# Kernel tuning notes

Hardware: AMD Instinct MI355X
Metric: run time of the kernel (lower is better)

## Reference

```python
import jax, jax.numpy as jnp
import numpy as np

B, S, H = 2, 2048, 768
NH, DH = 12, 64  # num_heads, dim_head; inner_dim = NH*DH = H
SCALE = DH ** -0.5


def setup_inputs() -> dict:
    key = jax.random.key(0)
    k1, k2, k3 = jax.random.split(key, 3)
    x = jax.random.normal(k1, (B, S, H), dtype=jnp.float32)
    w_qkv = jax.random.normal(k2, (3 * NH * DH, H), dtype=jnp.float32) * (H ** -0.5)
    w_out = jax.random.normal(k3, (H, NH * DH), dtype=jnp.float32) * ((NH * DH) ** -0.5)
    b_out = jnp.zeros((H,), dtype=jnp.float32)
    return {"x": x, "w_qkv": w_qkv, "w_out": w_out, "b_out": b_out}


def reference(x, w_qkv, w_out, b_out):
    b, s, _ = x.shape
    # qkv linear: [b, s, 3*inner]
    qkv = jnp.einsum('bsh,oh->bso', x, w_qkv)
    # 'b s (qkv l d) -> qkv b l s d'  (l = heads)
    qkv = qkv.reshape(b, s, 3, NH, DH).transpose(2, 0, 3, 1, 4)
    q, k, v = qkv[0], qkv[1], qkv[2]  # each [b, nh, s, dh]
    att = jax.nn.softmax(jnp.einsum('bhxd,bhyd->bhxy', q, k) * SCALE, axis=-1)
    out = jnp.einsum('bhxy,bhyd->bhxd', att, v)  # [b, nh, s, dh]
    out = out.transpose(0, 2, 1, 3).reshape(b, s, NH * DH)  # 'b h l d -> b l (h d)'
    return jnp.einsum('bsi,oi->bso', out, w_out) + b_out
```

## Files before the change

kernel.cpp:

```cpp
#include <hip/hip_runtime.h>
#include <cstdint>
#include <cstddef>

typedef __bf16 bf16;
typedef __bf16 bf16x8 __attribute__((ext_vector_type(8)));
typedef __bf16 bf16x4 __attribute__((ext_vector_type(4)));
typedef float  f32x4  __attribute__((ext_vector_type(4)));
typedef float  f32x16 __attribute__((ext_vector_type(16)));

constexpr int Bb  = 2;
constexpr int Ss  = 2048;
constexpr int Hh  = 768;
constexpr int NHh = 12;
constexpr int DHh = 64;
constexpr int Mm  = Bb * Ss;
constexpr int N3  = 3 * Hh;
constexpr int QKW = 2 * Hh;

__device__ __forceinline__ float fexp2(float x) { return __builtin_amdgcn_exp2f(x); }

__device__ __forceinline__ void gload_lds16(void* lds, const void* g) {
  __builtin_amdgcn_global_load_lds(
      (__attribute__((address_space(1))) void*)(uintptr_t)g,
      (__attribute__((address_space(3))) void*)(uint32_t)(uintptr_t)lds,
      16, 0, 0);
}

__global__ void cvt_f32_bf16(const float* __restrict__ in, bf16* __restrict__ out, int n4) {
  int i = blockIdx.x * blockDim.x + threadIdx.x;
  int st = gridDim.x * blockDim.x;
  for (; i < n4; i += st) {
    float4 v = ((const float4*)in)[i];
    bf16x4 o;
    o[0] = (bf16)v.x; o[1] = (bf16)v.y; o[2] = (bf16)v.z; o[3] = (bf16)v.w;
    ((bf16x4*)out)[i] = o;
  }
}

template<int CSTRIDE, int OUTMODE>
__global__ __launch_bounds__(256, 2)
void gemm_bt(const bf16* __restrict__ A, const bf16* __restrict__ Bw,
             bf16* __restrict__ Cb, bf16* __restrict__ VtG,
             float* __restrict__ Cf, const float* __restrict__ bias)
{
  constexpr int K = 768;
  __shared__ bf16 As[128 * 32];
  __shared__ bf16 Bs[128 * 32];
  const int tid  = threadIdx.x;
  const int wid  = tid >> 6, lane = tid & 63;
  const int lr   = lane & 15, lk = lane >> 4;
  const int n0   = blockIdx.x * 128, m0 = blockIdx.y * 128;
  const int wm   = (wid >> 1) * 64, wn = (wid & 1) * 64;

  f32x4 acc[4][4] = {};

  const char* Ag = (const char*)(A  + (size_t)m0 * K) + (size_t)(tid >> 2) * (K * 2) + (tid & 3) * 16;
  const char* Bg = (const char*)(Bw + (size_t)n0 * K) + (size_t)(tid >> 2) * (K * 2) + (tid & 3) * 16;
  char* AsW = (char*)As + wid * 1024;
  char* BsW = (char*)Bs + wid * 1024;
  constexpr size_t rstep = (size_t)64 * K * 2;

  for (int kb = 0; kb < K; kb += 32) {
    gload_lds16(AsW,        Ag + (size_t)kb * 2);
    gload_lds16(AsW + 4096, Ag + rstep + (size_t)kb * 2);
    gload_lds16(BsW,        Bg + (size_t)kb * 2);
    gload_lds16(BsW + 4096, Bg + rstep + (size_t)kb * 2);
    __syncthreads();
    bf16x8 af[4], bfv[4];
#pragma unroll
    for (int i = 0; i < 4; ++i) {
      af[i]  = *(const bf16x8*)((const char*)As + ((wm + i * 16 + lr) * 32 + lk * 8) * 2);
      bfv[i] = *(const bf16x8*)((const char*)Bs + ((wn + i * 16 + lr) * 32 + lk * 8) * 2);
    }
#pragma unroll
    for (int i = 0; i < 4; ++i)
#pragma unroll
      for (int j = 0; j < 4; ++j)
        acc[i][j] = __builtin_amdgcn_mfma_f32_16x16x32_bf16(af[i], bfv[j], acc[i][j], 0, 0, 0);
    __syncthreads();
  }

  if constexpr (OUTMODE == 1) {
#pragma unroll
    for (int i = 0; i < 4; ++i)
#pragma unroll
      for (int j = 0; j < 4; ++j) {
        const int n = n0 + wn + j * 16 + lr;
        const float bv = bias[n];
#pragma unroll
        for (int r = 0; r < 4; ++r) {
          const int m = m0 + wm + i * 16 + lk * 4 + r;
          Cf[(size_t)m * CSTRIDE + n] = acc[i][j][r] + bv;
        }
      }
  } else {
    if (n0 < QKW) {
#pragma unroll
      for (int i = 0; i < 4; ++i)
#pragma unroll
        for (int j = 0; j < 4; ++j) {
          const int n = n0 + wn + j * 16 + lr;
#pragma unroll
          for (int r = 0; r < 4; ++r) {
            const int m = m0 + wm + i * 16 + lk * 4 + r;
            Cb[(size_t)m * CSTRIDE + n] = (bf16)acc[i][j][r];
          }
        }
    } else {
      const int bidx = m0 >> 11;
      const int s0 = (m0 & 2047) + wm + lk * 4;
#pragma unroll
      for (int i = 0; i < 4; ++i)
#pragma unroll
        for (int j = 0; j < 4; ++j) {
          const int colv = (n0 - QKW) + wn + j * 16 + lr;
          const int hh = colv >> 6, dd = colv & 63;
          const int bh = bidx * NHh + hh;
          const int mb = s0 + i * 16;
          bf16x4 pv;
#pragma unroll
          for (int r = 0; r < 4; ++r) pv[r] = (bf16)acc[i][j][r];
          const size_t idx8 = (((size_t)bh * 128 + (mb >> 4)) * 2 + (dd >> 5)) * 64
                              + ((mb >> 3) & 1) * 32 + (dd & 31);
          *(bf16x4*)(VtG + idx8 * 8 + (mb & 7)) = pv;
        }
    }
  }
}

__global__ __launch_bounds__(256, 3)
void attn_fwd5(const bf16* __restrict__ qk, const bf16* __restrict__ Vfrag,
               bf16* __restrict__ aout)
{
  __shared__ __align__(16) char lds[32768];
  const int tid  = threadIdx.x;
  const int wid  = tid >> 6, lane = tid & 63;
  const int lq   = lane & 31, hi = lane >> 5;
  const int qh   = wid & 1, grp = wid >> 1;

  const int orig = blockIdx.x;
  const int swz  = (orig & 7) * 96 + (orig >> 3);
  const int qb   = swz & 31;
  const int bh   = swz >> 5;
  const int b    = bh / NHh, h = bh % NHh;
  const int q0   = qb * 64 + qh * 32;
  const int kvbase = grp * 1024;

  constexpr float Cs = 0.18033688011112042f;
  const bf16* qrow = qk + (size_t)(b * Ss + q0 + lq) * QKW + h * DHh;
  bf16x8 qf[4];
#pragma unroll
  for (int j = 0; j < 4; ++j) {
    bf16x8 t = *(const bf16x8*)(qrow + j * 16 + hi * 8);
#pragma unroll
    for (int e = 0; e < 8; ++e) t[e] = (bf16)((float)t[e] * Cs);
    qf[j] = t;
  }

  const int strow = qh * 32 + (lane >> 3);
  const int stcol = ((lane & 7) * 16) ^ (((lane >> 3) & 7) << 4);
  const char* Kg0 = (const char*)(qk + (size_t)(b * Ss) * QKW + Hh + h * DHh)
                    + (size_t)strow * (QKW * 2) + stcol;
  auto stageK = [&](int buf, int kvt) {
    char* db = lds + grp * 16384 + buf * 8192 + qh * 4096;
    const char* sg = Kg0 + (size_t)kvt * (QKW * 2);
#pragma unroll
    for (int c = 0; c < 4; ++c)
      gload_lds16(db + c * 1024, sg + (size_t)(c * 8) * (QKW * 2));
  };

  const char* Vf = (const char*)Vfrag + (size_t)bh * 262144 + lane * 16;

  f32x16 oacc[2] = {};
  f32x16 lacc = {};
  bf16x8 ones;
#pragma unroll
  for (int e = 0; e < 8; ++e) ones[e] = (bf16)1.0f;

  stageK(0, kvbase);
  asm volatile("s_waitcnt vmcnt(0)" ::: "memory");
  __builtin_amdgcn_sched_barrier(0);

#pragma unroll 1
  for (int i = 0; i < 16; ++i) {
    const int cur = i & 1;

    __builtin_amdgcn_s_barrier();

    bf16x8 vf[4][2];
    {
      const char* vp = Vf + (size_t)(grp * 64 + i * 4) * 2048;
#pragma unroll
      for (int s = 0; s < 4; ++s)
#pragma unroll
        for (int dc = 0; dc < 2; ++dc)
          vf[s][dc] = *(const bf16x8*)(vp + (s * 2 + dc) * 1024);
    }

    stageK(cur ^ 1, kvbase + ((i + 1) & 15) * 64);
    __builtin_amdgcn_sched_barrier(0);

    f32x16 sacc[2];
    __builtin_amdgcn_s_setprio(1);
#pragma unroll
    for (int kvc = 0; kvc < 2; ++kvc) {
      f32x16 s = {};
      const int row = kvc * 32 + lq;
      const char* kb = lds + grp * 16384 + cur * 8192 + row * 128;
      const int sw = (lq & 7) << 4;
#pragma unroll
      for (int j = 0; j < 4; ++j) {
        bf16x8 kf = *(const bf16x8*)(kb + ((j * 32 + hi * 16) ^ sw));
        s = __builtin_amdgcn_mfma_f32_32x32x16_bf16(kf, qf[j], s, 0, 0, 0);
      }
      sacc[kvc] = s;
    }
    __builtin_amdgcn_s_setprio(0);

    uint32_t w[2][8];
#pragma unroll
    for (int kvc = 0; kvc < 2; ++kvc)
#pragma unroll
      for (int m = 0; m < 8; ++m) {
        union { bf16 hh[2]; uint32_t u; } cv;
        cv.hh[0] = (bf16)fexp2(sacc[kvc][2 * m]);
        cv.hh[1] = (bf16)fexp2(sacc[kvc][2 * m + 1]);
        w[kvc][m] = cv.u;
      }

    asm volatile("s_waitcnt vmcnt(4)" ::: "memory");
    __builtin_amdgcn_sched_barrier(0);

    __builtin_amdgcn_s_setprio(1);
#pragma unroll
    for (int s = 0; s < 4; ++s) {
      const int kvc = s >> 1, sb = s & 1;
      uint32_t a0 = w[kvc][4 * sb + 0], b0 = w[kvc][4 * sb + 2];
      uint32_t a1 = w[kvc][4 * sb + 1], b1 = w[kvc][4 * sb + 3];
      asm("v_permlane32_swap_b32 %0, %1" : "+v"(a0), "+v"(b0));
      asm("v_permlane32_swap_b32 %0, %1" : "+v"(a1), "+v"(b1));
      union { uint32_t u[4]; bf16x8 v; } pf;
      pf.u[0] = a0; pf.u[1] = a1; pf.u[2] = b0; pf.u[3] = b1;
#pragma unroll
      for (int dc = 0; dc < 2; ++dc)
        oacc[dc] = __builtin_amdgcn_mfma_f32_32x32x16_bf16(vf[s][dc], pf.v, oacc[dc], 0, 0, 0);
      lacc = __builtin_amdgcn_mfma_f32_32x32x16_bf16(ones, pf.v, lacc, 0, 0, 0);
    }
    __builtin_amdgcn_s_setprio(0);

    asm volatile("s_waitcnt vmcnt(0)" ::: "memory");
    __builtin_amdgcn_sched_barrier(0);
  }

  __syncthreads();

  if (grp == 1) {
    char* mb = lds + qh * 8704;
#pragma unroll
    for (int dc = 0; dc < 2; ++dc)
#pragma unroll
      for (int rr = 0; rr < 4; ++rr) {
        f32x4 t;
#pragma unroll
        for (int e = 0; e < 4; ++e) t[e] = oacc[dc][rr * 4 + e];
        *(f32x4*)(mb + (dc * 4 + rr) * 1024 + lane * 16) = t;
      }
    *(float*)(mb + 8192 + lane * 4) = lacc[0];
  }
  __syncthreads();
  if (grp == 0) {
    const char* mb = lds + qh * 8704;
    const float l2 = *(const float*)(mb + 8192 + lane * 4);
    const float linv = 1.0f / (lacc[0] + l2);
    bf16* orow = aout + (size_t)(b * Ss + q0 + lq) * Hh + h * DHh;
#pragma unroll
    for (int dc = 0; dc < 2; ++dc)
#pragma unroll
      for (int rr = 0; rr < 4; ++rr) {
        const f32x4 o2 = *(const f32x4*)(mb + (dc * 4 + rr) * 1024 + lane * 16);
        bf16x4 ov;
#pragma unroll
        for (int e = 0; e < 4; ++e)
          ov[e] = (bf16)((oacc[dc][rr * 4 + e] + o2[e]) * linv);
        *(bf16x4*)(orow + dc * 32 + rr * 8 + hi * 4) = ov;
      }
  }
}

extern "C" void kernel_launch(void* const* d_in, const int* in_sizes, int n_in,
                              void* d_out, int out_size, void* d_ws, size_t ws_size,
                              hipStream_t stream) {
  const float* x     = (const float*)d_in[0];
  const float* w_qkv = (const float*)d_in[1];
  const float* w_out = (const float*)d_in[2];
  const float* b_out = (const float*)d_in[3];
  char* ws = (char*)d_ws;
  bf16* xb    = (bf16*)(ws + 0);
  bf16* wqkvb = (bf16*)(ws + 6291456);
  bf16* woutb = (bf16*)(ws + 9830400);
  bf16* qkb   = (bf16*)(ws + 11010048);
  bf16* VtG   = (bf16*)(ws + 23592960);
  bf16* aoutb = (bf16*)(ws + 29884416);

  cvt_f32_bf16<<<3072, 256, 0, stream>>>(x,     xb,    Mm * Hh / 4);
  cvt_f32_bf16<<<1728, 256, 0, stream>>>(w_qkv, wqkvb, N3 * Hh / 4);
  cvt_f32_bf16<<<576,  256, 0, stream>>>(w_out, woutb, Hh * Hh / 4);

  gemm_bt<QKW, 0><<<dim3(18, 32), 256, 0, stream>>>(xb, wqkvb, qkb, VtG, nullptr, nullptr);
  attn_fwd5<<<768, 256, 0, stream>>>(qkb, VtG, aoutb);
  gemm_bt<Hh, 1><<<dim3(6, 32), 256, 0, stream>>>(aoutb, woutb, nullptr, nullptr,
                                                  (float*)d_out, b_out);
}
```

Before: 98.02 us.

## Double-buffer GEMM LDS tiles, fuse conversion kernels, use BM=64 for output GEMM

The GEMM now double-buffers its LDS tiles, issuing the next k-slice's global-to-LDS loads before computing on the current one, which cuts one barrier per iteration and overlaps load latency with MFMA work. The three f32-to-bf16 conversion launches are merged into one kernel to save launch overhead. The output projection GEMM uses a 64-row tile, doubling its grid to 384 blocks for better CU occupancy. The cost is twice the LDS per block, and there is no explicit vmcnt wait before the barrier that follows the prefetch, which relies on the barrier ordering the async LDS loads.

Result: faster. 87.90 us (-10.3%).

```diff
diff --git a/kernel.cpp b/kernel.cpp
--- a/kernel.cpp
+++ b/kernel.cpp
@@ -26,63 +26,91 @@
       16, 0, 0);
 }
 
-__global__ void cvt_f32_bf16(const float* __restrict__ in, bf16* __restrict__ out, int n4) {
-  int i = blockIdx.x * blockDim.x + threadIdx.x;
-  int st = gridDim.x * blockDim.x;
-  for (; i < n4; i += st) {
-    float4 v = ((const float4*)in)[i];
-    bf16x4 o;
-    o[0] = (bf16)v.x; o[1] = (bf16)v.y; o[2] = (bf16)v.z; o[3] = (bf16)v.w;
-    ((bf16x4*)out)[i] = o;
-  }
-}
-
-template<int CSTRIDE, int OUTMODE>
+__global__ void cvt3_f32_bf16(const float* __restrict__ x,  bf16* __restrict__ xb,
+                              const float* __restrict__ w1, bf16* __restrict__ w1b,
+                              const float* __restrict__ w2, bf16* __restrict__ w2b) {
+  const int st = gridDim.x * blockDim.x;
+  int i0 = blockIdx.x * blockDim.x + threadIdx.x;
+  for (int i = i0; i < 786432; i += st) {
+    float4 v = ((const float4*)x)[i];
+    bf16x4 o; o[0]=(bf16)v.x; o[1]=(bf16)v.y; o[2]=(bf16)v.z; o[3]=(bf16)v.w;
+    ((bf16x4*)xb)[i] = o;
+  }
+  for (int i = i0; i < 442368; i += st) {
+    float4 v = ((const float4*)w1)[i];
+    bf16x4 o; o[0]=(bf16)v.x; o[1]=(bf16)v.y; o[2]=(bf16)v.z; o[3]=(bf16)v.w;
+    ((bf16x4*)w1b)[i] = o;
+  }
+  for (int i = i0; i < 147456; i += st) {
+    float4 v = ((const float4*)w2)[i];
+    bf16x4 o; o[0]=(bf16)v.x; o[1]=(bf16)v.y; o[2]=(bf16)v.z; o[3]=(bf16)v.w;
+    ((bf16x4*)w2b)[i] = o;
+  }
+}
+
+template<int CSTRIDE, int OUTMODE, int BM>
 __global__ __launch_bounds__(256, 2)
 void gemm_bt(const bf16* __restrict__ A, const bf16* __restrict__ Bw,
              bf16* __restrict__ Cb, bf16* __restrict__ VtG,
              float* __restrict__ Cf, const float* __restrict__ bias)
 {
   constexpr int K = 768;
-  __shared__ bf16 As[128 * 32];
-  __shared__ bf16 Bs[128 * 32];
+  constexpr int NT = K / 32;
+  constexpr int MI = BM / 32;
+  constexpr int ABUF = BM * 64;
+  __shared__ bf16 As[2][BM * 32];
+  __shared__ bf16 Bs[2][128 * 32];
   const int tid  = threadIdx.x;
   const int wid  = tid >> 6, lane = tid & 63;
   const int lr   = lane & 15, lk = lane >> 4;
-  const int n0   = blockIdx.x * 128, m0 = blockIdx.y * 128;
-  const int wm   = (wid >> 1) * 64, wn = (wid & 1) * 64;
-
-  f32x4 acc[4][4] = {};
+  const int n0   = blockIdx.x * 128, m0 = blockIdx.y * BM;
+  const int wm   = (wid >> 1) * (BM / 2), wn = (wid & 1) * 64;
+
+  f32x4 acc[MI][4] = {};
 
   const char* Ag = (const char*)(A  + (size_t)m0 * K) + (size_t)(tid >> 2) * (K * 2) + (tid & 3) * 16;
   const char* Bg = (const char*)(Bw + (size_t)n0 * K) + (size_t)(tid >> 2) * (K * 2) + (tid & 3) * 16;
-  char* AsW = (char*)As + wid * 1024;
-  char* BsW = (char*)Bs + wid * 1024;
   constexpr size_t rstep = (size_t)64 * K * 2;
 
-  for (int kb = 0; kb < K; kb += 32) {
-    gload_lds16(AsW,        Ag + (size_t)kb * 2);
-    gload_lds16(AsW + 4096, Ag + rstep + (size_t)kb * 2);
-    gload_lds16(BsW,        Bg + (size_t)kb * 2);
-    gload_lds16(BsW + 4096, Bg + rstep + (size_t)kb * 2);
-    __syncthreads();
-    bf16x8 af[4], bfv[4];
-#pragma unroll
-    for (int i = 0; i < 4; ++i) {
-      af[i]  = *(const bf16x8*)((const char*)As + ((wm + i * 16 + lr) * 32 + lk * 8) * 2);
-      bfv[i] = *(const bf16x8*)((const char*)Bs + ((wn + i * 16 + lr) * 32 + lk * 8) * 2);
-    }
-#pragma unroll
-    for (int i = 0; i < 4; ++i)
+  auto stage = [&](int buf, int kb) {
+    char* aw = (char*)As + buf * ABUF + wid * 1024;
+    char* bw = (char*)Bs + buf * 8192 + wid * 1024;
+    gload_lds16(aw, Ag + (size_t)kb * 2);
+    if constexpr (BM == 128)
+      gload_lds16(aw + 4096, Ag + rstep + (size_t)kb * 2);
+    gload_lds16(bw,        Bg + (size_t)kb * 2);
+    gload_lds16(bw + 4096, Bg + rstep + (size_t)kb * 2);
+  };
+
+  stage(0, 0);
+  asm volatile("s_waitcnt vmcnt(0)" ::: "memory");
+  __syncthreads();
+
+#pragma unroll 1
+  for (int t = 0; t < NT; ++t) {
+    const int cur = t & 1;
+    if (t + 1 < NT) stage(cur ^ 1, (t + 1) * 32);
+    __builtin_amdgcn_sched_barrier(0);
+
+    bf16x8 af[MI], bfv[4];
+#pragma unroll
+    for (int i = 0; i < MI; ++i)
+      af[i]  = *(const bf16x8*)((const char*)As + cur * ABUF + ((wm + i * 16 + lr) * 32 + lk * 8) * 2);
+#pragma unroll
+    for (int j = 0; j < 4; ++j)
+      bfv[j] = *(const bf16x8*)((const char*)Bs + cur * 8192 + ((wn + j * 16 + lr) * 32 + lk * 8) * 2);
+#pragma unroll
+    for (int i = 0; i < MI; ++i)
 #pragma unroll
       for (int j = 0; j < 4; ++j)
         acc[i][j] = __builtin_amdgcn_mfma_f32_16x16x32_bf16(af[i], bfv[j], acc[i][j], 0, 0, 0);
+
     __syncthreads();
   }
 
   if constexpr (OUTMODE == 1) {
 #pragma unroll
-    for (int i = 0; i < 4; ++i)
+    for (int i = 0; i < MI; ++i)
 #pragma unroll
       for (int j = 0; j < 4; ++j) {
         const int n = n0 + wn + j * 16 + lr;
@@ -96,7 +124,7 @@
   } else {
     if (n0 < QKW) {
 #pragma unroll
-      for (int i = 0; i < 4; ++i)
+      for (int i = 0; i < MI; ++i)
 #pragma unroll
         for (int j = 0; j < 4; ++j) {
           const int n = n0 + wn + j * 16 + lr;
@@ -110,7 +138,7 @@
       const int bidx = m0 >> 11;
       const int s0 = (m0 & 2047) + wm + lk * 4;
 #pragma unroll
-      for (int i = 0; i < 4; ++i)
+      for (int i = 0; i < MI; ++i)
 #pragma unroll
         for (int j = 0; j < 4; ++j) {
           const int colv = (n0 - QKW) + wn + j * 16 + lr;
@@ -299,15 +327,13 @@
   bf16* wqkvb = (bf16*)(ws + 6291456);
   bf16* woutb = (bf16*)(ws + 9830400);
   bf16* qkb   = (bf16*)(ws + 11010048);
-  bf16* VtG   = (bf16*)(ws + 23592960);
+  bf16* Vfrag = (bf16*)(ws + 23592960);
   bf16* aoutb = (bf16*)(ws + 29884416);
 
-  cvt_f32_bf16<<<3072, 256, 0, stream>>>(x,     xb,    Mm * Hh / 4);
-  cvt_f32_bf16<<<1728, 256, 0, stream>>>(w_qkv, wqkvb, N3 * Hh / 4);
-  cvt_f32_bf16<<<576,  256, 0, stream>>>(w_out, woutb, Hh * Hh / 4);
-
-  gemm_bt<QKW, 0><<<dim3(18, 32), 256, 0, stream>>>(xb, wqkvb, qkb, VtG, nullptr, nullptr);
-  attn_fwd5<<<768, 256, 0, stream>>>(qkb, VtG, aoutb);
-  gemm_bt<Hh, 1><<<dim3(6, 32), 256, 0, stream>>>(aoutb, woutb, nullptr, nullptr,
-                                                  (float*)d_out, b_out);
-}
+  cvt3_f32_bf16<<<2048, 256, 0, stream>>>(x, xb, w_qkv, wqkvb, w_out, woutb);
+
+  gemm_bt<QKW, 0, 128><<<dim3(18, 32), 256, 0, stream>>>(xb, wqkvb, qkb, Vfrag, nullptr, nullptr);
+  attn_fwd5<<<768, 256, 0, stream>>>(qkb, Vfrag, aoutb);
+  gemm_bt<Hh, 1, 64><<<dim3(6, 64), 256, 0, stream>>>(aoutb, woutb, nullptr, nullptr,
+                                                      (float*)d_out, b_out);
+}
```
